# Optimization experiments

Measured on AMD Instinct MI355X. Metric: run time of the kernel, lower is better.

## Reference

```python
import jax, jax.numpy as jnp
import numpy as np

N_VARS = 2048
N_LAYERS = 8
NODES = 4096
FAN_IN = 4
BATCH = 8192


def setup_inputs() -> dict:
    key = jax.random.key(0)
    k1, k2 = jax.random.split(key)
    x = jax.random.uniform(k1, (BATCH, N_VARS), dtype=jnp.float32)
    marginalized_variables = jnp.zeros((N_VARS,), dtype=bool)
    # child_idx[l, n, f]: index of the f-th child of node n in layer l,
    # pointing into the previous layer's 4096 outputs (leaves for l=0).
    child_idx = jax.random.randint(k2, (N_LAYERS, NODES, FAN_IN), 0, NODES, dtype=jnp.int64)
    return {"x": x, "marginalized_variables": marginalized_variables, "child_idx": child_idx}


def reference(x, marginalized_variables, child_idx):
    # Leaf literals: positive literal = x[:, v], negative literal = 1 - x[:, v].
    # Marginalized variables output 1.0 for both literals.
    leaves = jnp.concatenate([x, 1.0 - x], axis=1)            # [B, 2V]
    marg = jnp.tile(marginalized_variables, 2)                 # [2V]
    cur = jnp.where(marg[None, :], jnp.ones((), dtype=leaves.dtype), leaves)
    n_layers = child_idx.shape[0]
    for l in range(n_layers):  # fixed small layer loop; each layer fully vectorized
        gathered = cur[:, child_idx[l]]                        # [B, NODES, FAN_IN]
        if l % 2 == 0:  # AND layer: product of children
            cur = jnp.prod(gathered, axis=-1)                  # [B, NODES]
        else:            # OR layer: sum of children
            cur = jnp.sum(gathered, axis=-1)                   # [B, NODES]
    # Root OR node over the final layer -> [B, 1]
    return jnp.sum(cur, axis=1, keepdims=True)
```

## Files before the change

### kernel.cpp

```cpp
#include <hip/hip_runtime.h>

constexpr int N_VARS   = 2048;
constexpr int NODES    = 4096;
constexpr int N_LAYERS = 8;
constexpr int BATCH    = 8192;
constexpr int THREADS  = 256;
constexpr int RPB      = 2;
constexpr int NPT      = NODES / THREADS;

__device__ __forceinline__ float bflo(unsigned w) { return __uint_as_float(w << 16); }
__device__ __forceinline__ float bfhi(unsigned w) { return __uint_as_float(w & 0xffff0000u); }
__device__ __forceinline__ unsigned bfpack(float a, float b) {
  unsigned ua = __float_as_uint(a), ub = __float_as_uint(b);
  ua = (ua + 0x7fffu + ((ua >> 16) & 1u)) >> 16;
  ub = (ub + 0x7fffu + ((ub >> 16) & 1u)) & 0xffff0000u;
  return ua | ub;
}

template <int MODE>
__device__ __forceinline__ ushort4 get_idx(const void* p, int n) {
  if (MODE == 0) return ((const ushort4*)p)[n];
  if (MODE == 1) {
    int4 c = ((const int4*)p)[n];
    return make_ushort4((unsigned short)c.x, (unsigned short)c.y,
                        (unsigned short)c.z, (unsigned short)c.w);
  }
  const int* q = (const int*)p + (size_t)n * 8;
  return make_ushort4((unsigned short)q[0], (unsigned short)q[2],
                      (unsigned short)q[4], (unsigned short)q[6]);
}
template <int MODE> __device__ __forceinline__ size_t layer_bytes() {
  return MODE == 0 ? (size_t)NODES * 8 : MODE == 1 ? (size_t)NODES * 16
                                                   : (size_t)NODES * 32;
}

template <int MODE>
__device__ __forceinline__ void prod_pass(const float2* A, unsigned* B,
                                          const void* idx, int t) {
#pragma unroll
  for (int i = 0; i < NPT; ++i) {
    const int n = t + i * THREADS;
    ushort4 c = get_idx<MODE>(idx, n);
    float2 a = A[c.x], b = A[c.y], d = A[c.z], e = A[c.w];
    B[n] = bfpack(a.x * b.x * d.x * e.x, a.y * b.y * d.y * e.y);
  }
}

template <int MODE>
__device__ __forceinline__ void sum_pass(const unsigned* B, float2* A,
                                         const void* idx, int t) {
#pragma unroll
  for (int i = 0; i < NPT; ++i) {
    const int n = t + i * THREADS;
    ushort4 c = get_idx<MODE>(idx, n);
    unsigned a = B[c.x], b = B[c.y], d = B[c.z], e = B[c.w];
    A[n] = make_float2(bflo(a) + bflo(b) + bflo(d) + bflo(e),
                       bfhi(a) + bfhi(b) + bfhi(d) + bfhi(e));
  }
}

template <int MODE>
__device__ __forceinline__ void spn_body(const float* __restrict__ x,
                                         const unsigned char* __restrict__ marg,
                                         const void* __restrict__ idx,
                                         float* __restrict__ out,
                                         float2* A,
                                         unsigned* B) {
  const int t = threadIdx.x;
  const int row0 = blockIdx.x * RPB;
  const float* x0 = x + (size_t)row0 * N_VARS;
  const float* x1 = x0 + N_VARS;

#pragma unroll
  for (int i = 0; i < N_VARS / THREADS; ++i) {
    const int j = t + i * THREADS;
    const float a = x0[j], b = x1[j];
    const bool m = marg[j] != 0;
    A[j]          = make_float2(m ? 1.f : a,       m ? 1.f : b);
    A[N_VARS + j] = make_float2(m ? 1.f : 1.f - a, m ? 1.f : 1.f - b);
  }

  const char* ib = (const char*)idx;
  const size_t LB = layer_bytes<MODE>();
  __syncthreads();
  prod_pass<MODE>(A, B, ib + 0 * LB, t); __syncthreads();
  sum_pass <MODE>(B, A, ib + 1 * LB, t); __syncthreads();
  prod_pass<MODE>(A, B, ib + 2 * LB, t); __syncthreads();
  sum_pass <MODE>(B, A, ib + 3 * LB, t); __syncthreads();
  prod_pass<MODE>(A, B, ib + 4 * LB, t); __syncthreads();
  sum_pass <MODE>(B, A, ib + 5 * LB, t); __syncthreads();
  prod_pass<MODE>(A, B, ib + 6 * LB, t); __syncthreads();

  float s0 = 0.f, s1 = 0.f;
  {
    const void* L7 = ib + 7 * LB;
#pragma unroll
    for (int i = 0; i < NPT; ++i) {
      const int n = t + i * THREADS;
      ushort4 c = get_idx<MODE>(L7, n);
      unsigned a = B[c.x], b = B[c.y], d = B[c.z], e = B[c.w];
      s0 += bflo(a) + bflo(b) + bflo(d) + bflo(e);
      s1 += bfhi(a) + bfhi(b) + bfhi(d) + bfhi(e);
    }
  }
#pragma unroll
  for (int off = 32; off > 0; off >>= 1) {
    s0 += __shfl_down(s0, off);
    s1 += __shfl_down(s1, off);
  }
  if ((t & 63) == 0) A[t >> 6] = make_float2(s0, s1);
  __syncthreads();
  if (t == 0) {
    float2 tot = A[0];
#pragma unroll
    for (int w = 1; w < THREADS / 64; ++w) { tot.x += A[w].x; tot.y += A[w].y; }
    out[row0]     = tot.x;
    out[row0 + 1] = tot.y;
  }
}

__global__ __launch_bounds__(THREADS) void spn_packed(
    const float* __restrict__ x, const unsigned char* __restrict__ marg,
    const ushort4* __restrict__ idx, float* __restrict__ out) {
  __shared__ float2   A[NODES];
  __shared__ unsigned B[NODES];
  spn_body<0>(x, marg, idx, out, A, B);
}

__global__ __launch_bounds__(THREADS) void spn_raw(
    const float* __restrict__ x, const unsigned char* __restrict__ marg,
    const int* __restrict__ cidx, float* __restrict__ out) {
  __shared__ float2   A[NODES];
  __shared__ unsigned B[NODES];
  int acc = 0;
#pragma unroll
  for (int k = 0; k < 8; ++k) acc |= cidx[2 * k + 1];
  if (acc == 0) spn_body<2>(x, marg, cidx, out, A, B);
  else          spn_body<1>(x, marg, cidx, out, A, B);
}

__global__ void pack_idx(const int* __restrict__ cidx, ushort4* __restrict__ out) {
  const int g = blockIdx.x * blockDim.x + threadIdx.x;
  int acc = 0;
#pragma unroll
  for (int k = 0; k < 8; ++k) acc |= cidx[2 * k + 1];
  ushort4 r;
  if (acc == 0) {
    const int* p = cidx + (size_t)g * 8;
    r = make_ushort4((unsigned short)p[0], (unsigned short)p[2],
                     (unsigned short)p[4], (unsigned short)p[6]);
  } else {
    int4 c = ((const int4*)cidx)[g];
    r = make_ushort4((unsigned short)c.x, (unsigned short)c.y,
                     (unsigned short)c.z, (unsigned short)c.w);
  }
  out[g] = r;
}

extern "C" void kernel_launch(void* const* d_in, const int* in_sizes, int n_in,
                              void* d_out, int out_size, void* d_ws, size_t ws_size,
                              hipStream_t stream) {
  const float* x          = (const float*)d_in[0];
  const unsigned char* mg = (const unsigned char*)d_in[1];
  const int* cidx         = (const int*)d_in[2];
  float* out              = (float*)d_out;

  const size_t need = (size_t)N_LAYERS * NODES * sizeof(ushort4);
  if (ws_size >= need) {
    ushort4* packed = (ushort4*)d_ws;
    hipLaunchKernelGGL(pack_idx, dim3((N_LAYERS * NODES) / 256), dim3(256), 0, stream,
                       cidx, packed);
    hipLaunchKernelGGL(spn_packed, dim3(BATCH / RPB), dim3(THREADS), 0, stream,
                       x, mg, packed, out);
  } else {
    hipLaunchKernelGGL(spn_raw, dim3(BATCH / RPB), dim3(THREADS), 0, stream,
                       x, mg, cidx, out);
  }
}
```

Measured before the change: 202.0 us.

## Process four rows per block and reorder fan-in children to cut LDS bank conflicts

Each block now evaluates four batch rows, not two, using 512 threads. Node values are kept in LDS as float4 and packed bf16 uint2, so each random child gather serves four rows with one wide read. The index prep kernel becomes a per-layer pass that reorders each node's four children, balancing LDS bank usage across the 64 nodes a wavefront handles. This aims to reduce bank conflicts in the gathers. The cost is 96KB of dynamic LDS per block, which lowers block occupancy per CU, and a more serial prep kernel that runs on only 8 blocks.

```diff
diff --git a/kernel.cpp b/kernel.cpp
--- a/kernel.cpp
+++ b/kernel.cpp
@@ -4,9 +4,10 @@
 constexpr int NODES    = 4096;
 constexpr int N_LAYERS = 8;
 constexpr int BATCH    = 8192;
-constexpr int THREADS  = 256;
-constexpr int RPB      = 2;
+constexpr int THREADS  = 512;
+constexpr int RPB      = 4;
 constexpr int NPT      = NODES / THREADS;
+constexpr size_t SMEM  = (size_t)NODES * 16 + (size_t)NODES * 8;
 
 __device__ __forceinline__ float bflo(unsigned w) { return __uint_as_float(w << 16); }
 __device__ __forceinline__ float bfhi(unsigned w) { return __uint_as_float(w & 0xffff0000u); }
@@ -35,27 +36,30 @@
 }
 
 template <int MODE>
-__device__ __forceinline__ void prod_pass(const float2* A, unsigned* B,
+__device__ __forceinline__ void prod_pass(const float4* A, uint2* B,
                                           const void* idx, int t) {
 #pragma unroll
   for (int i = 0; i < NPT; ++i) {
     const int n = t + i * THREADS;
     ushort4 c = get_idx<MODE>(idx, n);
-    float2 a = A[c.x], b = A[c.y], d = A[c.z], e = A[c.w];
-    B[n] = bfpack(a.x * b.x * d.x * e.x, a.y * b.y * d.y * e.y);
-  }
-}
-
-template <int MODE>
-__device__ __forceinline__ void sum_pass(const unsigned* B, float2* A,
+    float4 a = A[c.x], b = A[c.y], d = A[c.z], e = A[c.w];
+    B[n] = make_uint2(bfpack(a.x * b.x * d.x * e.x, a.y * b.y * d.y * e.y),
+                      bfpack(a.z * b.z * d.z * e.z, a.w * b.w * d.w * e.w));
+  }
+}
+
+template <int MODE>
+__device__ __forceinline__ void sum_pass(const uint2* B, float4* A,
                                          const void* idx, int t) {
 #pragma unroll
   for (int i = 0; i < NPT; ++i) {
     const int n = t + i * THREADS;
     ushort4 c = get_idx<MODE>(idx, n);
-    unsigned a = B[c.x], b = B[c.y], d = B[c.z], e = B[c.w];
-    A[n] = make_float2(bflo(a) + bflo(b) + bflo(d) + bflo(e),
-                       bfhi(a) + bfhi(b) + bfhi(d) + bfhi(e));
+    uint2 a = B[c.x], b = B[c.y], d = B[c.z], e = B[c.w];
+    A[n] = make_float4(bflo(a.x) + bflo(b.x) + bflo(d.x) + bflo(e.x),
+                       bfhi(a.x) + bfhi(b.x) + bfhi(d.x) + bfhi(e.x),
+                       bflo(a.y) + bflo(b.y) + bflo(d.y) + bflo(e.y),
+                       bfhi(a.y) + bfhi(b.y) + bfhi(d.y) + bfhi(e.y));
   }
 }
 
@@ -64,20 +68,23 @@
                                          const unsigned char* __restrict__ marg,
                                          const void* __restrict__ idx,
                                          float* __restrict__ out,
-                                         float2* A,
-                                         unsigned* B) {
+                                         float4* A, uint2* B) {
   const int t = threadIdx.x;
   const int row0 = blockIdx.x * RPB;
   const float* x0 = x + (size_t)row0 * N_VARS;
   const float* x1 = x0 + N_VARS;
+  const float* x2 = x1 + N_VARS;
+  const float* x3 = x2 + N_VARS;
 
 #pragma unroll
   for (int i = 0; i < N_VARS / THREADS; ++i) {
     const int j = t + i * THREADS;
-    const float a = x0[j], b = x1[j];
+    float a0 = x0[j], a1 = x1[j], a2 = x2[j], a3 = x3[j];
     const bool m = marg[j] != 0;
-    A[j]          = make_float2(m ? 1.f : a,       m ? 1.f : b);
-    A[N_VARS + j] = make_float2(m ? 1.f : 1.f - a, m ? 1.f : 1.f - b);
+    if (m) { a0 = a1 = a2 = a3 = 1.f; }
+    A[j]          = make_float4(a0, a1, a2, a3);
+    A[N_VARS + j] = m ? make_float4(1.f, 1.f, 1.f, 1.f)
+                      : make_float4(1.f - a0, 1.f - a1, 1.f - a2, 1.f - a3);
   }
 
   const char* ib = (const char*)idx;
@@ -91,47 +98,55 @@
   sum_pass <MODE>(B, A, ib + 5 * LB, t); __syncthreads();
   prod_pass<MODE>(A, B, ib + 6 * LB, t); __syncthreads();
 
-  float s0 = 0.f, s1 = 0.f;
+  float s0 = 0.f, s1 = 0.f, s2 = 0.f, s3 = 0.f;
   {
     const void* L7 = ib + 7 * LB;
 #pragma unroll
     for (int i = 0; i < NPT; ++i) {
       const int n = t + i * THREADS;
       ushort4 c = get_idx<MODE>(L7, n);
-      unsigned a = B[c.x], b = B[c.y], d = B[c.z], e = B[c.w];
-      s0 += bflo(a) + bflo(b) + bflo(d) + bflo(e);
-      s1 += bfhi(a) + bfhi(b) + bfhi(d) + bfhi(e);
+      uint2 a = B[c.x], b = B[c.y], d = B[c.z], e = B[c.w];
+      s0 += bflo(a.x) + bflo(b.x) + bflo(d.x) + bflo(e.x);
+      s1 += bfhi(a.x) + bfhi(b.x) + bfhi(d.x) + bfhi(e.x);
+      s2 += bflo(a.y) + bflo(b.y) + bflo(d.y) + bflo(e.y);
+      s3 += bfhi(a.y) + bfhi(b.y) + bfhi(d.y) + bfhi(e.y);
     }
   }
 #pragma unroll
   for (int off = 32; off > 0; off >>= 1) {
     s0 += __shfl_down(s0, off);
     s1 += __shfl_down(s1, off);
-  }
-  if ((t & 63) == 0) A[t >> 6] = make_float2(s0, s1);
+    s2 += __shfl_down(s2, off);
+    s3 += __shfl_down(s3, off);
+  }
+  if ((t & 63) == 0) A[t >> 6] = make_float4(s0, s1, s2, s3);
   __syncthreads();
   if (t == 0) {
-    float2 tot = A[0];
-#pragma unroll
-    for (int w = 1; w < THREADS / 64; ++w) { tot.x += A[w].x; tot.y += A[w].y; }
-    out[row0]     = tot.x;
-    out[row0 + 1] = tot.y;
-  }
-}
-
-__global__ __launch_bounds__(THREADS) void spn_packed(
+    float4 tot = A[0];
+#pragma unroll
+    for (int w = 1; w < THREADS / 64; ++w) {
+      float4 p = A[w];
+      tot.x += p.x; tot.y += p.y; tot.z += p.z; tot.w += p.w;
+    }
+    ((float4*)out)[blockIdx.x] = tot;
+  }
+}
+
+extern __shared__ char smem[];
+
+__global__ __launch_bounds__(THREADS) void spn_packed4(
     const float* __restrict__ x, const unsigned char* __restrict__ marg,
     const ushort4* __restrict__ idx, float* __restrict__ out) {
-  __shared__ float2   A[NODES];
-  __shared__ unsigned B[NODES];
+  float4* A = (float4*)smem;
+  uint2*  B = (uint2*)(smem + NODES * 16);
   spn_body<0>(x, marg, idx, out, A, B);
 }
 
-__global__ __launch_bounds__(THREADS) void spn_raw(
+__global__ __launch_bounds__(THREADS) void spn_raw4(
     const float* __restrict__ x, const unsigned char* __restrict__ marg,
     const int* __restrict__ cidx, float* __restrict__ out) {
-  __shared__ float2   A[NODES];
-  __shared__ unsigned B[NODES];
+  float4* A = (float4*)smem;
+  uint2*  B = (uint2*)(smem + NODES * 16);
   int acc = 0;
 #pragma unroll
   for (int k = 0; k < 8; ++k) acc |= cidx[2 * k + 1];
@@ -139,22 +154,75 @@
   else          spn_body<1>(x, marg, cidx, out, A, B);
 }
 
-__global__ void pack_idx(const int* __restrict__ cidx, ushort4* __restrict__ out) {
-  const int g = blockIdx.x * blockDim.x + threadIdx.x;
+__global__ __launch_bounds__(64) void prep_idx(const int* __restrict__ cidx,
+                                               ushort4* __restrict__ out) {
+  __shared__ ushort4  idxbuf[64][65];
+  __shared__ unsigned hist[64][17];
+  const int l = blockIdx.x;
+  const int t = threadIdx.x;
+
   int acc = 0;
 #pragma unroll
   for (int k = 0; k < 8; ++k) acc |= cidx[2 * k + 1];
-  ushort4 r;
-  if (acc == 0) {
-    const int* p = cidx + (size_t)g * 8;
-    r = make_ushort4((unsigned short)p[0], (unsigned short)p[2],
-                     (unsigned short)p[4], (unsigned short)p[6]);
-  } else {
-    int4 c = ((const int4*)cidx)[g];
-    r = make_ushort4((unsigned short)c.x, (unsigned short)c.y,
-                     (unsigned short)c.z, (unsigned short)c.w);
-  }
-  out[g] = r;
+  const bool i64 = (acc == 0);
+
+  const size_t lbase = (size_t)l * NODES;
+  for (int g = 0; g < 64; ++g) {
+    const size_t n = lbase + g * 64 + t;
+    ushort4 r;
+    if (i64) {
+      const int4* p = (const int4*)cidx + n * 2;
+      int4 u = p[0], v = p[1];
+      r = make_ushort4((unsigned short)u.x, (unsigned short)u.z,
+                       (unsigned short)v.x, (unsigned short)v.z);
+    } else {
+      int4 u = ((const int4*)cidx)[n];
+      r = make_ushort4((unsigned short)u.x, (unsigned short)u.y,
+                       (unsigned short)u.z, (unsigned short)u.w);
+    }
+    idxbuf[g][t] = r;
+  }
+#pragma unroll
+  for (int b = 0; b < 17; ++b) hist[t][b] = 0;
+  __syncthreads();
+
+  const int mask = ((l & 1) == 0) ? 7 : 15;
+  unsigned* h = hist[t];
+  for (int lane = 0; lane < 64; ++lane) {
+    ushort4 c = idxbuf[t][lane];
+    unsigned short v[4] = {c.x, c.y, c.z, c.w};
+    int bank[4]; unsigned wv[4];
+#pragma unroll
+    for (int k = 0; k < 4; ++k) bank[k] = v[k] & mask;
+#pragma unroll
+    for (int k = 0; k < 4; ++k) wv[k] = h[bank[k]];
+    int slot[4]; unsigned used = 0;
+    unsigned short o[4];
+#pragma unroll
+    for (int k = 0; k < 4; ++k) {
+      unsigned eff = wv[k];
+#pragma unroll
+      for (int j = 0; j < 4; ++j)
+        if (j < k && bank[j] == bank[k]) eff += 1u << (8 * slot[j]);
+      const unsigned m2 = eff | used;
+      int best = 0; unsigned bv = m2 & 0xffu;
+#pragma unroll
+      for (int s = 1; s < 4; ++s) {
+        const unsigned q = (m2 >> (8 * s)) & 0xffu;
+        if (q < bv) { bv = q; best = s; }
+      }
+      slot[k] = best; used |= 0xffu << (8 * best); o[best] = v[k];
+    }
+#pragma unroll
+    for (int k = 0; k < 4; ++k) {
+      unsigned fin = wv[k];
+#pragma unroll
+      for (int j = 0; j < 4; ++j)
+        if (bank[j] == bank[k]) fin += 1u << (8 * slot[j]);
+      h[bank[k]] = fin;
+    }
+    out[lbase + t * 64 + lane] = make_ushort4(o[0], o[1], o[2], o[3]);
+  }
 }
 
 extern "C" void kernel_launch(void* const* d_in, const int* in_sizes, int n_in,
@@ -165,15 +233,19 @@
   const int* cidx         = (const int*)d_in[2];
   float* out              = (float*)d_out;
 
+  (void)hipFuncSetAttribute((const void*)spn_packed4,
+                            hipFuncAttributeMaxDynamicSharedMemorySize, (int)SMEM);
+  (void)hipFuncSetAttribute((const void*)spn_raw4,
+                            hipFuncAttributeMaxDynamicSharedMemorySize, (int)SMEM);
+
   const size_t need = (size_t)N_LAYERS * NODES * sizeof(ushort4);
   if (ws_size >= need) {
     ushort4* packed = (ushort4*)d_ws;
-    hipLaunchKernelGGL(pack_idx, dim3((N_LAYERS * NODES) / 256), dim3(256), 0, stream,
-                       cidx, packed);
-    hipLaunchKernelGGL(spn_packed, dim3(BATCH / RPB), dim3(THREADS), 0, stream,
+    hipLaunchKernelGGL(prep_idx, dim3(N_LAYERS), dim3(64), 0, stream, cidx, packed);
+    hipLaunchKernelGGL(spn_packed4, dim3(BATCH / RPB), dim3(THREADS), SMEM, stream,
                        x, mg, packed, out);
   } else {
-    hipLaunchKernelGGL(spn_raw, dim3(BATCH / RPB), dim3(THREADS), 0, stream,
+    hipLaunchKernelGGL(spn_raw4, dim3(BATCH / RPB), dim3(THREADS), SMEM, stream,
                        x, mg, cidx, out);
   }
 }
```

Result: slower. 222.9 us (+10.4%).

## Reorder child indices to balance LDS bank conflicts and use 1024-thread blocks

Applied to the files above, without the earlier changes.

The index-packing kernel now runs one wavefront per 64 nodes. For each node it permutes the four child indices so that, at each of the four gather steps, the lanes spread their LDS accesses across banks more evenly, using a greedy per-slot bank histogram. Because AND and OR are commutative, reordering children within a node leaves the result unchanged. The main kernel moves from 256 to 1024 threads per block with a launch-bounds occupancy hint, and the two row outputs are written as one float2 store. The prep kernel is serial over 64 iterations, so it adds some fixed cost. The 1024-thread block size together with the occupancy hint may also limit registers per thread.

```diff
diff --git a/kernel.cpp b/kernel.cpp
--- a/kernel.cpp
+++ b/kernel.cpp
@@ -4,7 +4,7 @@
 constexpr int NODES    = 4096;
 constexpr int N_LAYERS = 8;
 constexpr int BATCH    = 8192;
-constexpr int THREADS  = 256;
+constexpr int THREADS  = 1024;
 constexpr int RPB      = 2;
 constexpr int NPT      = NODES / THREADS;
 
@@ -114,12 +114,11 @@
     float2 tot = A[0];
 #pragma unroll
     for (int w = 1; w < THREADS / 64; ++w) { tot.x += A[w].x; tot.y += A[w].y; }
-    out[row0]     = tot.x;
-    out[row0 + 1] = tot.y;
-  }
-}
-
-__global__ __launch_bounds__(THREADS) void spn_packed(
+    ((float2*)out)[blockIdx.x] = tot;
+  }
+}
+
+__global__ __launch_bounds__(THREADS, 8) void spn_packed(
     const float* __restrict__ x, const unsigned char* __restrict__ marg,
     const ushort4* __restrict__ idx, float* __restrict__ out) {
   __shared__ float2   A[NODES];
@@ -127,7 +126,7 @@
   spn_body<0>(x, marg, idx, out, A, B);
 }
 
-__global__ __launch_bounds__(THREADS) void spn_raw(
+__global__ __launch_bounds__(THREADS, 8) void spn_raw(
     const float* __restrict__ x, const unsigned char* __restrict__ marg,
     const int* __restrict__ cidx, float* __restrict__ out) {
   __shared__ float2   A[NODES];
@@ -139,22 +138,69 @@
   else          spn_body<1>(x, marg, cidx, out, A, B);
 }
 
-__global__ void pack_idx(const int* __restrict__ cidx, ushort4* __restrict__ out) {
-  const int g = blockIdx.x * blockDim.x + threadIdx.x;
+__global__ __launch_bounds__(64) void prep_idx(const int* __restrict__ cidx,
+                                               ushort4* __restrict__ out) {
+  const int gid  = blockIdx.x;
+  const int l    = gid >> 6;
+  const int cgrp = gid & 63;
+  const int lane = threadIdx.x;
+  const size_t n = (size_t)l * NODES + cgrp * 64 + lane;
+
   int acc = 0;
 #pragma unroll
   for (int k = 0; k < 8; ++k) acc |= cidx[2 * k + 1];
+
   ushort4 r;
   if (acc == 0) {
-    const int* p = cidx + (size_t)g * 8;
-    r = make_ushort4((unsigned short)p[0], (unsigned short)p[2],
-                     (unsigned short)p[4], (unsigned short)p[6]);
+    const int4* p = (const int4*)cidx + n * 2;
+    int4 u = p[0], v = p[1];
+    r = make_ushort4((unsigned short)u.x, (unsigned short)u.z,
+                     (unsigned short)v.x, (unsigned short)v.z);
   } else {
-    int4 c = ((const int4*)cidx)[g];
-    r = make_ushort4((unsigned short)c.x, (unsigned short)c.y,
-                     (unsigned short)c.z, (unsigned short)c.w);
-  }
-  out[g] = r;
+    int4 u = ((const int4*)cidx)[n];
+    r = make_ushort4((unsigned short)u.x, (unsigned short)u.y,
+                     (unsigned short)u.z, (unsigned short)u.w);
+  }
+  const unsigned w0 = (unsigned)r.x | ((unsigned)r.y << 16);
+  const unsigned w1 = (unsigned)r.z | ((unsigned)r.w << 16);
+  const int mask = ((l & 1) == 0) ? 15 : 31;
+
+  unsigned hcnt = 0;
+  ushort4 mine = r;
+  for (int k = 0; k < 64; ++k) {
+    const unsigned a0 = __shfl(w0, k);
+    const unsigned a1 = __shfl(w1, k);
+    unsigned short v4[4] = {(unsigned short)(a0 & 0xffffu), (unsigned short)(a0 >> 16),
+                            (unsigned short)(a1 & 0xffffu), (unsigned short)(a1 >> 16)};
+    int bank[4];
+#pragma unroll
+    for (int j = 0; j < 4; ++j) bank[j] = v4[j] & mask;
+    unsigned cnt[4];
+#pragma unroll
+    for (int j = 0; j < 4; ++j) cnt[j] = __shfl(hcnt, bank[j]);
+    int slot[4]; unsigned used = 0;
+    unsigned short o[4];
+#pragma unroll
+    for (int j = 0; j < 4; ++j) {
+      unsigned eff = cnt[j];
+#pragma unroll
+      for (int p2 = 0; p2 < 4; ++p2)
+        if (p2 < j && bank[p2] == bank[j]) eff += 1u << (8 * slot[p2]);
+      const unsigned m2 = eff | used;
+      int best = 0; unsigned bv = m2 & 0xffu;
+#pragma unroll
+      for (int s = 1; s < 4; ++s) {
+        const unsigned q = (m2 >> (8 * s)) & 0xffu;
+        if (q < bv) { bv = q; best = s; }
+      }
+      slot[j] = best; used |= 0xffu << (8 * best); o[best] = v4[j];
+    }
+#pragma unroll
+    for (int j = 0; j < 4; ++j)
+      if (lane == bank[j]) hcnt += 1u << (8 * slot[j]);
+    if (lane == k) mine = make_ushort4(o[0], o[1], o[2], o[3]);
+  }
+  out[n] = mine;
 }
 
 extern "C" void kernel_launch(void* const* d_in, const int* in_sizes, int n_in,
@@ -168,7 +214,7 @@
   const size_t need = (size_t)N_LAYERS * NODES * sizeof(ushort4);
   if (ws_size >= need) {
     ushort4* packed = (ushort4*)d_ws;
-    hipLaunchKernelGGL(pack_idx, dim3((N_LAYERS * NODES) / 256), dim3(256), 0, stream,
+    hipLaunchKernelGGL(prep_idx, dim3(N_LAYERS * 64), dim3(64), 0, stream,
                        cidx, packed);
     hipLaunchKernelGGL(spn_packed, dim3(BATCH / RPB), dim3(THREADS), 0, stream,
                        x, mg, packed, out);
```

Result: slower. 212.7 us (+5.3%).
